# Performance work log

Hardware: AMD Instinct MI355X
Metric: run time of the kernel (lower is better)

## Reference

```python
import jax, jax.numpy as jnp
import numpy as np

MAXDISP = 48
GROUP = 8
EPS = 1e-5


def setup_inputs() -> dict:
    key = jax.random.key(0)
    k1, k2 = jax.random.split(key)
    x = jax.random.normal(k1, (2, 64, 96, 320), dtype=jnp.float32)
    y = jax.random.normal(k2, (2, 64, 96, 320), dtype=jnp.float32)
    return {"x": x, "y": y}


def reference(x, y):
    # Faithful translation of CostVolume.forward.
    # torch's unfold over left-zero-padded y at kernel position d picks
    # y_pad[..., j + d]; per-window L2 norm over channels reduces to a
    # per-pixel channel norm (padded zeros normalize to zero), so we
    # normalize once and gather shifted columns.
    D = MAXDISP + 1
    b, c, h, w = x.shape
    cpg = c // GROUP
    xg = x.reshape(b, GROUP, cpg, h, w)
    yg = y.reshape(b, GROUP, cpg, h, w)
    xn = xg / (jnp.linalg.norm(xg, axis=2, keepdims=True) + EPS)
    yn = yg / (jnp.linalg.norm(yg, axis=2, keepdims=True) + EPS)
    # left zero-pad width dim by MAXDISP (padded zeros stay zero after norm)
    y_pad = jnp.pad(yn, ((0, 0), (0, 0), (0, 0), (0, 0), (MAXDISP, 0)))
    # after torch.flip on the disparity axis, disparity k compares x[:, j]
    # with y[:, j - k]  ->  padded index j + MAXDISP - k
    idx = jnp.arange(w)[None, :] + MAXDISP - jnp.arange(D)[:, None]  # [D, w]
    y_shift = y_pad[..., idx]  # [b, g, cpg, h, D, w]
    cost = jnp.sum(jnp.abs(xn[:, :, :, :, None, :] - y_shift), axis=2)  # [b,g,h,D,w]
    return jnp.transpose(cost, (0, 1, 3, 2, 4))  # [b, group, D, h, w]
```

## Files before the change

### kernel.cpp

```cpp
#include <hip/hip_runtime.h>


#define HH   96
#define WW   320
#define HW   (HH * WW)
#define NDISP 49
#define EPSN 1e-5f

__global__ __launch_bounds__(WW) void cost_volume_kernel(
    const float* __restrict__ x, const float* __restrict__ y,
    float* __restrict__ out)
{
    __shared__ float xn_s[8][WW];
    __shared__ float yn_s[8][WW];

    const int t   = threadIdx.x;
    const int blk = blockIdx.x;
    const int h   = blk % HH;
    const int bg  = blk / HH;

    const size_t inBase = (size_t)bg * 8 * HW + (size_t)h * WW;

    {
        float xv[8], yv[8];
        float xs = 0.f, ys = 0.f;
#pragma unroll
        for (int cc = 0; cc < 8; ++cc) {
            float xi = x[inBase + (size_t)cc * HW + t];
            float yi = y[inBase + (size_t)cc * HW + t];
            xv[cc] = xi; yv[cc] = yi;
            xs += xi * xi;
            ys += yi * yi;
        }
        const float xinv = 1.f / (sqrtf(xs) + EPSN);
        const float yinv = 1.f / (sqrtf(ys) + EPSN);
#pragma unroll
        for (int cc = 0; cc < 8; ++cc) {
            xn_s[cc][t] = xv[cc] * xinv;
            yn_s[cc][t] = yv[cc] * yinv;
        }
    }
    __syncthreads();

    const int q  = t % 80;
    const int dc = t / 80;
    const int Q  = q * 4;

    float4 xq[8];
#pragma unroll
    for (int cc = 0; cc < 8; ++cc)
        xq[cc] = *(const float4*)&xn_s[cc][Q];

    float4 sA = make_float4(0.f, 0.f, 0.f, 0.f);
#pragma unroll
    for (int cc = 0; cc < 8; ++cc) {
        sA.x += fabsf(xq[cc].x);
        sA.y += fabsf(xq[cc].y);
        sA.z += fabsf(xq[cc].z);
        sA.w += fabsf(xq[cc].w);
    }

    const int g0 = (dc == 0) ? 0 : (3 * dc + 1);
    const int g1 = 3 * dc + 4;

    float* outp = out + (size_t)bg * (NDISP * HW) + (size_t)h * WW + Q;

    for (int g = g0; g < g1; ++g) {
        int wq0 = q - g - 1; if (wq0 < 0) wq0 = 0;
        int wq1 = q - g;     if (wq1 < 0) wq1 = 0;
        const int a0 = wq0 * 4, a1 = wq1 * 4;

        float acc[4][4];
#pragma unroll
        for (int e = 0; e < 4; ++e)
#pragma unroll
            for (int k = 0; k < 4; ++k) acc[e][k] = 0.f;

#pragma unroll
        for (int cc = 0; cc < 8; ++cc) {
            const float4 wa = *(const float4*)&yn_s[cc][a0];
            const float4 wb = *(const float4*)&yn_s[cc][a1];
            const float win[8] = { wa.x, wa.y, wa.z, wa.w,
                                   wb.x, wb.y, wb.z, wb.w };
            const float4 xc = xq[cc];
#pragma unroll
            for (int e = 0; e < 4; ++e) {
                acc[e][0] += fabsf(xc.x - win[4 - e]);
                acc[e][1] += fabsf(xc.y - win[5 - e]);
                acc[e][2] += fabsf(xc.z - win[6 - e]);
                acc[e][3] += fabsf(xc.w - win[7 - e]);
            }
        }

#pragma unroll
        for (int e = 0; e < 4; ++e) {
            const int d = 4 * g + e;
            float4 r;
            r.x = (Q + 0 < d) ? sA.x : acc[e][0];
            r.y = (Q + 1 < d) ? sA.y : acc[e][1];
            r.z = (Q + 2 < d) ? sA.z : acc[e][2];
            r.w = (Q + 3 < d) ? sA.w : acc[e][3];
            if (d < NDISP)
                *(float4*)&outp[(size_t)d * HW] = r;
        }
    }
}

extern "C" void kernel_launch(void* const* d_in, const int* in_sizes, int n_in,
                              void* d_out, int out_size, void* d_ws, size_t ws_size,
                              hipStream_t stream) {
    const float* x = (const float*)d_in[0];
    const float* y = (const float*)d_in[1];
    float* out = (float*)d_out;
    dim3 grid(2 * 8 * HH);
    dim3 block(WW);
    cost_volume_kernel<<<grid, block, 0, stream>>>(x, y, out);
}
```

Before: 138.0 us.

## Process three rows per block with each thread covering all disparities

Before, each block handled one image row and split the 13 disparity groups across four thread slices. Now each block handles three rows, each thread computes all 13 disparity groups for one 4-column quad, and the normalization phase loads inputs as float4. The aim is fewer, larger blocks and vectorized input loads, cutting per-block launch and sync overhead. In exchange the grid shrinks to 512 blocks and each thread does more serial work, which could reduce occupancy and latency hiding on a device with many CUs.

```diff
diff --git a/kernel.cpp b/kernel.cpp
--- a/kernel.cpp
+++ b/kernel.cpp
@@ -1,74 +1,90 @@
 #include <hip/hip_runtime.h>
 
 
-#define HH   96
-#define WW   320
-#define HW   (HH * WW)
+#define HH    96
+#define WW    320
+#define HW    (HH * WW)
 #define NDISP 49
-#define EPSN 1e-5f
+#define EPSN  1e-5f
+#define ROWS  3
+#define QR    (WW / 4)
+#define NT    (ROWS * QR)
+#define NC    (ROWS * WW)
 
-__global__ __launch_bounds__(WW) void cost_volume_kernel(
+__global__ __launch_bounds__(NT) void cost_volume_kernel(
     const float* __restrict__ x, const float* __restrict__ y,
     float* __restrict__ out)
 {
-    __shared__ float xn_s[8][WW];
-    __shared__ float yn_s[8][WW];
+    __shared__ float xn_s[8][NC];
+    __shared__ float yn_s[8][NC];
 
     const int t   = threadIdx.x;
     const int blk = blockIdx.x;
-    const int h   = blk % HH;
-    const int bg  = blk / HH;
+    const int hb  = blk % (HH / ROWS);
+    const int bg  = blk / (HH / ROWS);
+    const int h0  = hb * ROWS;
 
-    const size_t inBase = (size_t)bg * 8 * HW + (size_t)h * WW;
+    const size_t base = (size_t)bg * 8 * HW + (size_t)h0 * WW;
 
     {
-        float xv[8], yv[8];
-        float xs = 0.f, ys = 0.f;
+        const int c = 4 * t;
+        float4 xa[8], ya[8];
 #pragma unroll
         for (int cc = 0; cc < 8; ++cc) {
-            float xi = x[inBase + (size_t)cc * HW + t];
-            float yi = y[inBase + (size_t)cc * HW + t];
-            xv[cc] = xi; yv[cc] = yi;
-            xs += xi * xi;
-            ys += yi * yi;
+            xa[cc] = *(const float4*)&x[base + (size_t)cc * HW + c];
+            ya[cc] = *(const float4*)&y[base + (size_t)cc * HW + c];
         }
-        const float xinv = 1.f / (sqrtf(xs) + EPSN);
-        const float yinv = 1.f / (sqrtf(ys) + EPSN);
+        float4 xs = make_float4(0.f, 0.f, 0.f, 0.f);
+        float4 ys = make_float4(0.f, 0.f, 0.f, 0.f);
 #pragma unroll
         for (int cc = 0; cc < 8; ++cc) {
-            xn_s[cc][t] = xv[cc] * xinv;
-            yn_s[cc][t] = yv[cc] * yinv;
+            xs.x += xa[cc].x * xa[cc].x;  xs.y += xa[cc].y * xa[cc].y;
+            xs.z += xa[cc].z * xa[cc].z;  xs.w += xa[cc].w * xa[cc].w;
+            ys.x += ya[cc].x * ya[cc].x;  ys.y += ya[cc].y * ya[cc].y;
+            ys.z += ya[cc].z * ya[cc].z;  ys.w += ya[cc].w * ya[cc].w;
+        }
+        const float4 xi = make_float4(1.f / (sqrtf(xs.x) + EPSN),
+                                      1.f / (sqrtf(xs.y) + EPSN),
+                                      1.f / (sqrtf(xs.z) + EPSN),
+                                      1.f / (sqrtf(xs.w) + EPSN));
+        const float4 yi = make_float4(1.f / (sqrtf(ys.x) + EPSN),
+                                      1.f / (sqrtf(ys.y) + EPSN),
+                                      1.f / (sqrtf(ys.z) + EPSN),
+                                      1.f / (sqrtf(ys.w) + EPSN));
+#pragma unroll
+        for (int cc = 0; cc < 8; ++cc) {
+            *(float4*)&xn_s[cc][c] = make_float4(xa[cc].x * xi.x, xa[cc].y * xi.y,
+                                                 xa[cc].z * xi.z, xa[cc].w * xi.w);
+            *(float4*)&yn_s[cc][c] = make_float4(ya[cc].x * yi.x, ya[cc].y * yi.y,
+                                                 ya[cc].z * yi.z, ya[cc].w * yi.w);
         }
     }
     __syncthreads();
 
-    const int q  = t % 80;
-    const int dc = t / 80;
-    const int Q  = q * 4;
+    const int q = t % QR;
+    const int r = t / QR;
+    const int Q = 4 * q;
+    const int rowOff = r * WW;
 
     float4 xq[8];
 #pragma unroll
     for (int cc = 0; cc < 8; ++cc)
-        xq[cc] = *(const float4*)&xn_s[cc][Q];
+        xq[cc] = *(const float4*)&xn_s[cc][rowOff + Q];
 
     float4 sA = make_float4(0.f, 0.f, 0.f, 0.f);
 #pragma unroll
     for (int cc = 0; cc < 8; ++cc) {
-        sA.x += fabsf(xq[cc].x);
-        sA.y += fabsf(xq[cc].y);
-        sA.z += fabsf(xq[cc].z);
-        sA.w += fabsf(xq[cc].w);
+        sA.x += fabsf(xq[cc].x);  sA.y += fabsf(xq[cc].y);
+        sA.z += fabsf(xq[cc].z);  sA.w += fabsf(xq[cc].w);
     }
 
-    const int g0 = (dc == 0) ? 0 : (3 * dc + 1);
-    const int g1 = 3 * dc + 4;
+    float* outp = out + (size_t)bg * (NDISP * HW) + (size_t)(h0 + r) * WW + Q;
 
-    float* outp = out + (size_t)bg * (NDISP * HW) + (size_t)h * WW + Q;
-
-    for (int g = g0; g < g1; ++g) {
+    for (int g = 0; g < 13; ++g) {
         int wq0 = q - g - 1; if (wq0 < 0) wq0 = 0;
         int wq1 = q - g;     if (wq1 < 0) wq1 = 0;
-        const int a0 = wq0 * 4, a1 = wq1 * 4;
+        const int a0 = rowOff + 4 * wq0;
+        const int a1 = rowOff + 4 * wq1;
 
         float acc[4][4];
 #pragma unroll
@@ -95,13 +111,14 @@
 #pragma unroll
         for (int e = 0; e < 4; ++e) {
             const int d = 4 * g + e;
-            float4 r;
-            r.x = (Q + 0 < d) ? sA.x : acc[e][0];
-            r.y = (Q + 1 < d) ? sA.y : acc[e][1];
-            r.z = (Q + 2 < d) ? sA.z : acc[e][2];
-            r.w = (Q + 3 < d) ? sA.w : acc[e][3];
-            if (d < NDISP)
-                *(float4*)&outp[(size_t)d * HW] = r;
+            if (d < NDISP) {
+                float4 rr;
+                rr.x = (Q + 0 < d) ? sA.x : acc[e][0];
+                rr.y = (Q + 1 < d) ? sA.y : acc[e][1];
+                rr.z = (Q + 2 < d) ? sA.z : acc[e][2];
+                rr.w = (Q + 3 < d) ? sA.w : acc[e][3];
+                *(float4*)&outp[(size_t)d * HW] = rr;
+            }
         }
     }
 }
@@ -112,7 +129,7 @@
     const float* x = (const float*)d_in[0];
     const float* y = (const float*)d_in[1];
     float* out = (float*)d_out;
-    dim3 grid(2 * 8 * HH);
-    dim3 block(WW);
+    dim3 grid(16 * (HH / ROWS));
+    dim3 block(NT);
     cost_volume_kernel<<<grid, block, 0, stream>>>(x, y, out);
 }
```

New measurement: 140.0 us. About the same (+1.4%).

## Remap threads so each wave covers 16 columns across all disparity groups

Applied to the files above, without the earlier changes.

Threads are remapped so each 64-lane wavefront holds 16 column-quads times 4 disparity chunks, instead of splitting disparity chunks by t/80. Each chunk now does exactly 3 groups in a fully unrolled loop. The leftover disparity 48 is computed by every lane in a separate tail step, but only dc==0 lanes store it. The aim is to remove the uneven loop trip count and divergence and to balance work, with a launch-bounds occupancy hint added. The cost is redundant tail computation in three of every four lanes.

```diff
diff --git a/kernel.cpp b/kernel.cpp
--- a/kernel.cpp
+++ b/kernel.cpp
@@ -1,13 +1,13 @@
 #include <hip/hip_runtime.h>
 
 
-#define HH   96
-#define WW   320
-#define HW   (HH * WW)
+#define HH    96
+#define WW    320
+#define HW    (HH * WW)
 #define NDISP 49
-#define EPSN 1e-5f
+#define EPSN  1e-5f
 
-__global__ __launch_bounds__(WW) void cost_volume_kernel(
+__global__ __launch_bounds__(WW, 4) void cost_volume_kernel(
     const float* __restrict__ x, const float* __restrict__ y,
     float* __restrict__ out)
 {
@@ -19,15 +19,15 @@
     const int h   = blk % HH;
     const int bg  = blk / HH;
 
-    const size_t inBase = (size_t)bg * 8 * HW + (size_t)h * WW;
+    const size_t base = (size_t)bg * 8 * HW + (size_t)h * WW;
 
     {
         float xv[8], yv[8];
         float xs = 0.f, ys = 0.f;
 #pragma unroll
         for (int cc = 0; cc < 8; ++cc) {
-            float xi = x[inBase + (size_t)cc * HW + t];
-            float yi = y[inBase + (size_t)cc * HW + t];
+            float xi = x[base + (size_t)cc * HW + t];
+            float yi = y[base + (size_t)cc * HW + t];
             xv[cc] = xi; yv[cc] = yi;
             xs += xi * xi;
             ys += yi * yi;
@@ -42,9 +42,11 @@
     }
     __syncthreads();
 
-    const int q  = t % 80;
-    const int dc = t / 80;
-    const int Q  = q * 4;
+    const int w  = t >> 6;
+    const int l  = t & 63;
+    const int q  = w * 16 + (l & 15);
+    const int dc = l >> 4;
+    const int Q  = 4 * q;
 
     float4 xq[8];
 #pragma unroll
@@ -54,21 +56,19 @@
     float4 sA = make_float4(0.f, 0.f, 0.f, 0.f);
 #pragma unroll
     for (int cc = 0; cc < 8; ++cc) {
-        sA.x += fabsf(xq[cc].x);
-        sA.y += fabsf(xq[cc].y);
-        sA.z += fabsf(xq[cc].z);
-        sA.w += fabsf(xq[cc].w);
+        sA.x += fabsf(xq[cc].x);  sA.y += fabsf(xq[cc].y);
+        sA.z += fabsf(xq[cc].z);  sA.w += fabsf(xq[cc].w);
     }
-
-    const int g0 = (dc == 0) ? 0 : (3 * dc + 1);
-    const int g1 = 3 * dc + 4;
 
     float* outp = out + (size_t)bg * (NDISP * HW) + (size_t)h * WW + Q;
 
-    for (int g = g0; g < g1; ++g) {
+#pragma unroll
+    for (int gi = 0; gi < 3; ++gi) {
+        const int g = 3 * dc + gi;
         int wq0 = q - g - 1; if (wq0 < 0) wq0 = 0;
         int wq1 = q - g;     if (wq1 < 0) wq1 = 0;
-        const int a0 = wq0 * 4, a1 = wq1 * 4;
+        const int a0 = 4 * wq0;
+        const int a1 = 4 * wq1;
 
         float acc[4][4];
 #pragma unroll
@@ -95,14 +95,34 @@
 #pragma unroll
         for (int e = 0; e < 4; ++e) {
             const int d = 4 * g + e;
-            float4 r;
-            r.x = (Q + 0 < d) ? sA.x : acc[e][0];
-            r.y = (Q + 1 < d) ? sA.y : acc[e][1];
-            r.z = (Q + 2 < d) ? sA.z : acc[e][2];
-            r.w = (Q + 3 < d) ? sA.w : acc[e][3];
-            if (d < NDISP)
-                *(float4*)&outp[(size_t)d * HW] = r;
+            float4 rr;
+            rr.x = (Q + 0 < d) ? sA.x : acc[e][0];
+            rr.y = (Q + 1 < d) ? sA.y : acc[e][1];
+            rr.z = (Q + 2 < d) ? sA.z : acc[e][2];
+            rr.w = (Q + 3 < d) ? sA.w : acc[e][3];
+            *(float4*)&outp[(size_t)d * HW] = rr;
         }
+    }
+
+    {
+        int wq = q - 12; if (wq < 0) wq = 0;
+        const int a = 4 * wq;
+        float4 acc = make_float4(0.f, 0.f, 0.f, 0.f);
+#pragma unroll
+        for (int cc = 0; cc < 8; ++cc) {
+            const float4 wv = *(const float4*)&yn_s[cc][a];
+            acc.x += fabsf(xq[cc].x - wv.x);
+            acc.y += fabsf(xq[cc].y - wv.y);
+            acc.z += fabsf(xq[cc].z - wv.z);
+            acc.w += fabsf(xq[cc].w - wv.w);
+        }
+        float4 rr;
+        rr.x = (Q + 0 < 48) ? sA.x : acc.x;
+        rr.y = (Q + 1 < 48) ? sA.y : acc.y;
+        rr.z = (Q + 2 < 48) ? sA.z : acc.z;
+        rr.w = (Q + 3 < 48) ? sA.w : acc.w;
+        if (dc == 0)
+            *(float4*)&outp[(size_t)48 * HW] = rr;
     }
 }
 
@@ -112,7 +132,7 @@
     const float* x = (const float*)d_in[0];
     const float* y = (const float*)d_in[1];
     float* out = (float*)d_out;
-    dim3 grid(2 * 8 * HH);
+    dim3 grid(16 * HH);
     dim3 block(WW);
     cost_volume_kernel<<<grid, block, 0, stream>>>(x, y, out);
 }
```

Result: faster. 131.5 us (-4.8%).
